# Optimization experiments

Measured on AMD Instinct MI355X. Metric: run time of the kernel, lower is better.

Reference implementation:

```python
import jax, jax.numpy as jnp
import numpy as np

N_EMBD = 768
N_HEAD = 12
HEAD_DIM = N_EMBD // N_HEAD


def setup_inputs() -> dict:
    key = jax.random.key(0)
    k1, k2, k3 = jax.random.split(key, 3)
    B, T, C = 4, 2048, N_EMBD
    x = jax.random.normal(k1, (B, T, C), dtype=jnp.float32)
    # c_attn: torch Linear(C, 3C) -> store as (C, 3C) for x @ W
    w_attn = jax.random.normal(k2, (C, 3 * C), dtype=jnp.float32) * (1.0 / np.sqrt(C))
    b_attn = jax.random.normal(k3, (3 * C,), dtype=jnp.float32) * 0.02
    return {"x": x, "w_attn": w_attn, "b_attn": b_attn}


def reference(x, w_attn, b_attn):
    B, T, C = x.shape
    H, D = N_HEAD, HEAD_DIM
    scale = 1.0 / np.sqrt(D).astype(np.float32)

    qkv = x @ w_attn + b_attn                      # (B, T, 3C)
    q, k, v = jnp.split(qkv, 3, axis=-1)
    q = q.reshape(B, T, H, D).transpose(0, 2, 1, 3)  # (B, H, T, D)
    k = k.reshape(B, T, H, D).transpose(0, 2, 1, 3)
    v = v.reshape(B, T, H, D).transpose(0, 2, 1, 3)

    att = jnp.einsum('bhid,bhjd->bhij', q, k) * scale  # (B, H, T, T)
    causal = jnp.tril(jnp.ones((T, T), dtype=bool))
    # masked positions -> -inf -> relu -> 0; kept positions -> relu(scaled score)
    att = jnp.where(causal, jnp.maximum(att, 0.0), 0.0)

    y = jnp.einsum('bhij,bhjd->bhid', att, v)      # (B, H, T, D)
    y = y.transpose(0, 2, 1, 3).reshape(B, T, C)
    return y
```

## Files before the change

### kernel.cpp

```cpp
#include <hip/hip_runtime.h>
#include <hip/hip_bf16.h>

typedef short bf16x8 __attribute__((ext_vector_type(8)));
typedef float f32x4  __attribute__((ext_vector_type(4)));
typedef unsigned short u16x4 __attribute__((ext_vector_type(4)));

#define CDIM   768
#define NQKV   2304
#define MROWS  8192
#define TSEQ   2048
#define HD     64
#define NHEAD  12
#define BHTOT  48

__device__ __forceinline__ unsigned short f2bf(float f) {
    unsigned int x;
    __builtin_memcpy(&x, &f, 4);
    unsigned int r = (x + 0x7fffu + ((x >> 16) & 1u)) >> 16;
    return (unsigned short)r;
}

__device__ __forceinline__ unsigned int pkbf(float a, float b) {
    unsigned int ua, ub;
    __builtin_memcpy(&ua, &a, 4);
    __builtin_memcpy(&ub, &b, 4);
    return __builtin_amdgcn_perm(ua + 0x8000u, ub + 0x8000u, 0x03020706u);
}

__device__ __forceinline__ f32x4 mfma16(bf16x8 a, bf16x8 b, f32x4 c) {
    return __builtin_amdgcn_mfma_f32_16x16x32_bf16(a, b, c, 0, 0, 0);
}

__device__ __forceinline__ void gl_lds16(const unsigned short* g, unsigned short* l) {
    __builtin_amdgcn_global_load_lds(
        (__attribute__((address_space(1))) void*)(g),
        (__attribute__((address_space(3))) void*)(l),
        16, 0, 0);
}

__global__ __launch_bounds__(256) void convert_x(
    const float* __restrict__ X, unsigned short* __restrict__ Xb)
{
    size_t i = ((size_t)blockIdx.x * 256 + threadIdx.x) * 4;
    f32x4 v = *(const f32x4*)(X + i);
    u16x4 o;
#pragma unroll
    for (int j = 0; j < 4; j++) o[j] = f2bf(v[j]);
    *(u16x4*)(Xb + i) = o;
}

__global__ __launch_bounds__(256) void transpose_w(
    const float* __restrict__ W, unsigned short* __restrict__ Wt)
{
    __shared__ __align__(16) unsigned short tile[64][72];
    const int bx = blockIdx.x;
    const int by = blockIdx.y;
    const int tid = threadIdx.x;
#pragma unroll
    for (int c = 0; c < 4; c++) {
        int chunk = tid + 256 * c;
        int r = chunk >> 4, cc = chunk & 15;
        f32x4 v = *(const f32x4*)(W + (size_t)(by * 64 + r) * NQKV + bx * 64 + cc * 4);
#pragma unroll
        for (int j = 0; j < 4; j++) tile[cc * 4 + j][r] = f2bf(v[j]);
    }
    __syncthreads();
#pragma unroll
    for (int c = 0; c < 2; c++) {
        int chunk = tid + 256 * c;
        int r = chunk >> 3, cc = chunk & 7;
        bf16x8 v;
#pragma unroll
        for (int j = 0; j < 8; j++) v[j] = (short)tile[r][cc * 8 + j];
        *(bf16x8*)(Wt + (size_t)(bx * 64 + r) * CDIM + by * 64 + cc * 8) = v;
    }
}

#define BM 128
#define BN 128
#define BK 64

__global__ __launch_bounds__(256, 4) void qkv_gemm(
    const unsigned short* __restrict__ X,
    const unsigned short* __restrict__ Wt,
    const float* __restrict__ Bias,
    unsigned short* __restrict__ Q,
    unsigned short* __restrict__ Km,
    unsigned short* __restrict__ Vt)
{
    __shared__ __align__(16) unsigned short As[BM * BK];
    __shared__ __align__(16) unsigned short Bs[BN * BK];
    const int tid  = threadIdx.x;
    const int wave = tid >> 6, lane = tid & 63;
    const int quad = lane >> 4, m16 = lane & 15;
    const int wr = wave >> 1, wc = wave & 1;
    const int m0 = blockIdx.y * BM, n0 = blockIdx.x * BN;

    f32x4 acc[4][4];
#pragma unroll
    for (int i = 0; i < 4; i++)
#pragma unroll
        for (int j = 0; j < 4; j++) acc[i][j] = f32x4{0.f, 0.f, 0.f, 0.f};

    const unsigned short* xb = X + (size_t)m0 * CDIM;
    const unsigned short* wb = Wt + (size_t)n0 * CDIM;

    const int srow[4] = {
        (wave * 256 + 0 * 64 + lane) >> 3, (wave * 256 + 1 * 64 + lane) >> 3,
        (wave * 256 + 2 * 64 + lane) >> 3, (wave * 256 + 3 * 64 + lane) >> 3 };
    const int spos = lane & 7;
    const int rb = m16 & 7;

    for (int k0 = 0; k0 < CDIM; k0 += BK) {
#pragma unroll
        for (int c = 0; c < 4; c++) {
            int row = srow[c];
            int ch = spos ^ (row & 7);
            gl_lds16(xb + (size_t)row * CDIM + k0 + ch * 8, As + wave * 2048 + c * 512);
            gl_lds16(wb + (size_t)row * CDIM + k0 + ch * 8, Bs + wave * 2048 + c * 512);
        }
        __syncthreads();
#pragma unroll
        for (int ks = 0; ks < 2; ks++) {
            bf16x8 af[4], bfg[4];
#pragma unroll
            for (int t = 0; t < 4; t++) {
                int rowa = wr * 64 + t * 16 + m16;
                int rowb = wc * 64 + t * 16 + m16;
                int pos = (ks * 4 + quad) ^ rb;
                af[t]  = *(const bf16x8*)(As + rowa * 64 + pos * 8);
                bfg[t] = *(const bf16x8*)(Bs + rowb * 64 + pos * 8);
            }
#pragma unroll
            for (int i = 0; i < 4; i++)
#pragma unroll
                for (int j = 0; j < 4; j++)
                    acc[i][j] = mfma16(af[i], bfg[j], acc[i][j]);
        }
        __syncthreads();
    }

    const int region = n0 / CDIM;
    const float qscale = (region == 0) ? 0.125f : 1.0f;
#pragma unroll
    for (int i = 0; i < 4; i++) {
        int row = m0 + wr * 64 + i * 16 + quad * 4;
#pragma unroll
        for (int j = 0; j < 4; j++) {
            int gcol = n0 + wc * 64 + j * 16 + m16;
            int cc = gcol - region * CDIM;
            int h = cc >> 6, d = cc & 63;
            float bv = Bias[gcol];
#pragma unroll
            for (int r = 0; r < 4; r++) {
                int gm = row + r;
                int b = gm >> 11, t = gm & 2047;
                int bh = b * NHEAD + h;
                unsigned short o = f2bf((acc[i][j][r] + bv) * qscale);
                if (region == 0)      Q[((size_t)bh * TSEQ + t) * HD + d] = o;
                else if (region == 1) Km[((size_t)bh * TSEQ + t) * HD + d] = o;
                else                  Vt[((size_t)bh * HD + d) * TSEQ + t] = o;
            }
        }
    }
}

#define LDSK 0
#define LDSV 8192

__global__ __launch_bounds__(256, 4) void attn(
    const unsigned short* __restrict__ Q,
    const unsigned short* __restrict__ Kmat,
    const unsigned short* __restrict__ Vt,
    float* __restrict__ Out)
{
    __shared__ __align__(16) unsigned short S[16384];

    const int tid  = threadIdx.x;
    const int wave = tid >> 6, lane = tid & 63;
    const int q4 = lane >> 4, m16 = lane & 15;
    const int q8 = m16 >> 2, m3 = m16 & 3;

    const int xcd = blockIdx.x & 7;
    const int idx = blockIdx.x >> 3;
    const int bh  = xcd * 6 + (idx % 6);
    const int it  = 15 - (idx / 6);
    const int i0  = it * 128;

    const unsigned short* qb = Q    + (size_t)bh * TSEQ * HD;
    const unsigned short* kb = Kmat + (size_t)bh * TSEQ * HD;
    const unsigned short* vb = Vt   + (size_t)bh * HD * TSEQ;

    bf16x8 qf[2][2];
#pragma unroll
    for (int si = 0; si < 2; si++)
#pragma unroll
        for (int ks = 0; ks < 2; ks++)
            qf[si][ks] = *(const bf16x8*)(qb +
                (size_t)(i0 + wave * 32 + si * 16 + m16) * HD + ks * 32 + q4 * 8);

    f32x4 oacc[2][4];
#pragma unroll
    for (int si = 0; si < 2; si++)
#pragma unroll
        for (int dn = 0; dn < 4; dn++) oacc[si][dn] = f32x4{0.f, 0.f, 0.f, 0.f};

    const int fr  = ((q8 & 1) << 2) | m3;
    const int kx0 = (q4 ^ fr) * 8;
    const int kx1 = kx0 ^ 32;
    const int krb = (q8 * 8 + m3) * 64;

    for (int jt = 0; jt <= it; jt++) {
        const int j0 = jt * 128;
#pragma unroll
        for (int cc = 0; cc < 4; cc++) {
            int cs = wave * 4 + cc;
            {
                int rowK = cs * 8 + (lane >> 3);
                int chK  = (lane & 7) ^ ((((rowK >> 3) & 1) << 2) | (rowK & 3));
                gl_lds16(kb + (size_t)(j0 + rowK) * HD + chK * 8, &S[LDSK] + cs * 512);
            }
            {
                int dV  = cs * 4 + (lane >> 4);
                int chV = (m16 & 8) | ((m16 ^ dV) & 7);
                gl_lds16(vb + (size_t)dV * TSEQ + j0 + chV * 8, &S[LDSV] + cs * 512);
            }
        }
        __syncthreads();

        const bool diag = (jt == it);
#pragma unroll
        for (int kk = 0; kk < 4; kk++) {
            const int kb0 = kk * 2048 + krb;
            bf16x8 kf_e0 = *(const bf16x8*)(&S[LDSK] + kb0 + kx0);
            bf16x8 kf_e1 = *(const bf16x8*)(&S[LDSK] + kb0 + kx1);
            bf16x8 kf_o0 = *(const bf16x8*)(&S[LDSK] + kb0 + 256 + kx0);
            bf16x8 kf_o1 = *(const bf16x8*)(&S[LDSK] + kb0 + 256 + kx1);

            f32x4 sacc[2][2];
#pragma unroll
            for (int o = 0; o < 2; o++)
#pragma unroll
                for (int si = 0; si < 2; si++) sacc[o][si] = f32x4{0.f, 0.f, 0.f, 0.f};
#pragma unroll
            for (int si = 0; si < 2; si++) {
                sacc[0][si] = mfma16(kf_e0, qf[si][0], sacc[0][si]);
                sacc[0][si] = mfma16(kf_e1, qf[si][1], sacc[0][si]);
                sacc[1][si] = mfma16(kf_o0, qf[si][0], sacc[1][si]);
                sacc[1][si] = mfma16(kf_o1, qf[si][1], sacc[1][si]);
            }

            unsigned int pk[2][2][2];
#pragma unroll
            for (int o = 0; o < 2; o++)
#pragma unroll
                for (int si = 0; si < 2; si++) {
                    f32x4 v = sacc[o][si];
                    if (diag) {
#pragma unroll
                        for (int r = 0; r < 4; r++) {
                            int gj = kk * 32 + q4 * 8 + o * 4 + r;
                            int gi = wave * 32 + si * 16 + m16;
                            if (gj > gi) v[r] = 0.f;
                        }
                    }
#pragma unroll
                    for (int r = 0; r < 4; r++) v[r] = fmaxf(v[r], 0.f);
                    pk[o][si][0] = pkbf(v[0], v[1]);
                    pk[o][si][1] = pkbf(v[2], v[3]);
                }

#pragma unroll
            for (int dn = 0; dn < 4; dn++) {
                int vsw = ((kk * 4 + q4) ^ (m16 & 7)) * 8;
                bf16x8 vf = *(const bf16x8*)(&S[LDSV] + (dn * 16 + m16) * 128 + vsw);
#pragma unroll
                for (int si = 0; si < 2; si++) {
                    union { bf16x8 v; unsigned int u[4]; } af;
                    af.u[0] = pk[0][si][0];
                    af.u[1] = pk[0][si][1];
                    af.u[2] = pk[1][si][0];
                    af.u[3] = pk[1][si][1];
                    oacc[si][dn] = mfma16(af.v, vf, oacc[si][dn]);
                }
            }
        }
        __syncthreads();
    }

    const int b = bh / NHEAD, h = bh % NHEAD;
#pragma unroll
    for (int si = 0; si < 2; si++) {
        int ri = i0 + wave * 32 + si * 16 + q4 * 4;
#pragma unroll
        for (int dn = 0; dn < 4; dn++) {
            int d = dn * 16 + m16;
#pragma unroll
            for (int r = 0; r < 4; r++) {
                Out[((size_t)b * TSEQ + ri + r) * CDIM + h * HD + d] = oacc[si][dn][r];
            }
        }
    }
}

extern "C" void kernel_launch(void* const* d_in, const int* in_sizes, int n_in,
                              void* d_out, int out_size, void* d_ws, size_t ws_size,
                              hipStream_t stream) {
    const float* X    = (const float*)d_in[0];
    const float* W    = (const float*)d_in[1];
    const float* Bias = (const float*)d_in[2];
    float* out = (float*)d_out;

    unsigned short* Xb = (unsigned short*)d_ws;
    unsigned short* Wt = Xb + (size_t)MROWS * CDIM;
    unsigned short* Q  = Wt + (size_t)NQKV * CDIM;
    unsigned short* Km = Q  + (size_t)BHTOT * TSEQ * HD;
    unsigned short* Vt = Km + (size_t)BHTOT * TSEQ * HD;

    hipLaunchKernelGGL(convert_x, dim3((MROWS * CDIM) / 1024), dim3(256), 0, stream, X, Xb);
    hipLaunchKernelGGL(transpose_w, dim3(NQKV / 64, CDIM / 64), dim3(256), 0, stream, W, Wt);
    hipLaunchKernelGGL(qkv_gemm, dim3(NQKV / BN, MROWS / BM), dim3(256), 0, stream,
                       Xb, Wt, Bias, Q, Km, Vt);
    hipLaunchKernelGGL(attn, dim3(BHTOT * 16), dim3(256), 0, stream, Q, Km, Vt, out);
}
```

Baseline: 182.1 us.

## Fuse all stages into one persistent kernel with grid-wide atomic barriers

Merges the input conversion, weight transpose, QKV GEMM and causal attention into a single persistent kernel of 512 blocks, separated by atomic-counter grid barriers instead of separate launches. The attention stage pairs a long and a short query tile in each block so the triangular work is spread more evenly across the fixed grid. This is meant to remove launch gaps and tail imbalance. In exchange it lowers occupancy with launch_bounds(256,2), adds spin-barrier cost, and depends on all 512 blocks being resident at once or the barrier deadlocks.

```diff
diff --git a/kernel.cpp b/kernel.cpp
--- a/kernel.cpp
+++ b/kernel.cpp
@@ -12,6 +12,7 @@
 #define HD     64
 #define NHEAD  12
 #define BHTOT  48
+#define NBLK   512
 
 __device__ __forceinline__ unsigned short f2bf(float f) {
     unsigned int x;
@@ -38,266 +39,281 @@
         16, 0, 0);
 }
 
-__global__ __launch_bounds__(256) void convert_x(
-    const float* __restrict__ X, unsigned short* __restrict__ Xb)
+__device__ __forceinline__ void gbar(unsigned int* ctr) {
+    __syncthreads();
+    if (threadIdx.x == 0) {
+        __threadfence();
+        __hip_atomic_fetch_add(ctr, 1u, __ATOMIC_RELEASE, __HIP_MEMORY_SCOPE_AGENT);
+        while (__hip_atomic_load(ctr, __ATOMIC_ACQUIRE, __HIP_MEMORY_SCOPE_AGENT) <
+               (unsigned)NBLK)
+            __builtin_amdgcn_s_sleep(1);
+        __threadfence();
+    }
+    __syncthreads();
+}
+
+__global__ __launch_bounds__(256, 2) void mega(
+    const float* __restrict__ X, const float* __restrict__ W,
+    const float* __restrict__ Bias, unsigned int* __restrict__ bar,
+    unsigned short* __restrict__ Xb, unsigned short* __restrict__ Wt,
+    unsigned short* __restrict__ Q, unsigned short* __restrict__ Km,
+    unsigned short* __restrict__ Vt, float* __restrict__ Out)
 {
-    size_t i = ((size_t)blockIdx.x * 256 + threadIdx.x) * 4;
-    f32x4 v = *(const f32x4*)(X + i);
-    u16x4 o;
-#pragma unroll
-    for (int j = 0; j < 4; j++) o[j] = f2bf(v[j]);
-    *(u16x4*)(Xb + i) = o;
-}
-
-__global__ __launch_bounds__(256) void transpose_w(
-    const float* __restrict__ W, unsigned short* __restrict__ Wt)
-{
-    __shared__ __align__(16) unsigned short tile[64][72];
-    const int bx = blockIdx.x;
-    const int by = blockIdx.y;
-    const int tid = threadIdx.x;
-#pragma unroll
-    for (int c = 0; c < 4; c++) {
-        int chunk = tid + 256 * c;
-        int r = chunk >> 4, cc = chunk & 15;
-        f32x4 v = *(const f32x4*)(W + (size_t)(by * 64 + r) * NQKV + bx * 64 + cc * 4);
-#pragma unroll
-        for (int j = 0; j < 4; j++) tile[cc * 4 + j][r] = f2bf(v[j]);
-    }
-    __syncthreads();
-#pragma unroll
-    for (int c = 0; c < 2; c++) {
-        int chunk = tid + 256 * c;
-        int r = chunk >> 3, cc = chunk & 7;
-        bf16x8 v;
-#pragma unroll
-        for (int j = 0; j < 8; j++) v[j] = (short)tile[r][cc * 8 + j];
-        *(bf16x8*)(Wt + (size_t)(bx * 64 + r) * CDIM + by * 64 + cc * 8) = v;
-    }
-}
-
-#define BM 128
-#define BN 128
-#define BK 64
-
-__global__ __launch_bounds__(256, 4) void qkv_gemm(
-    const unsigned short* __restrict__ X,
-    const unsigned short* __restrict__ Wt,
-    const float* __restrict__ Bias,
-    unsigned short* __restrict__ Q,
-    unsigned short* __restrict__ Km,
-    unsigned short* __restrict__ Vt)
-{
-    __shared__ __align__(16) unsigned short As[BM * BK];
-    __shared__ __align__(16) unsigned short Bs[BN * BK];
+    __shared__ __align__(16) unsigned short SH[16384];
+
     const int tid  = threadIdx.x;
+    const int blk  = blockIdx.x;
     const int wave = tid >> 6, lane = tid & 63;
     const int quad = lane >> 4, m16 = lane & 15;
-    const int wr = wave >> 1, wc = wave & 1;
-    const int m0 = blockIdx.y * BM, n0 = blockIdx.x * BN;
-
-    f32x4 acc[4][4];
-#pragma unroll
-    for (int i = 0; i < 4; i++)
-#pragma unroll
-        for (int j = 0; j < 4; j++) acc[i][j] = f32x4{0.f, 0.f, 0.f, 0.f};
-
-    const unsigned short* xb = X + (size_t)m0 * CDIM;
-    const unsigned short* wb = Wt + (size_t)n0 * CDIM;
-
-    const int srow[4] = {
-        (wave * 256 + 0 * 64 + lane) >> 3, (wave * 256 + 1 * 64 + lane) >> 3,
-        (wave * 256 + 2 * 64 + lane) >> 3, (wave * 256 + 3 * 64 + lane) >> 3 };
-    const int spos = lane & 7;
-    const int rb = m16 & 7;
-
-    for (int k0 = 0; k0 < CDIM; k0 += BK) {
+
+    if (blk < 432) {
+        unsigned short (*tile)[72] = (unsigned short (*)[72])SH;
+        const int bx = blk % 36, by = blk / 36;
 #pragma unroll
         for (int c = 0; c < 4; c++) {
-            int row = srow[c];
-            int ch = spos ^ (row & 7);
-            gl_lds16(xb + (size_t)row * CDIM + k0 + ch * 8, As + wave * 2048 + c * 512);
-            gl_lds16(wb + (size_t)row * CDIM + k0 + ch * 8, Bs + wave * 2048 + c * 512);
+            int chunk = tid + 256 * c;
+            int r = chunk >> 4, cc = chunk & 15;
+            f32x4 v = *(const f32x4*)(W + (size_t)(by * 64 + r) * NQKV + bx * 64 + cc * 4);
+#pragma unroll
+            for (int j = 0; j < 4; j++) tile[cc * 4 + j][r] = f2bf(v[j]);
         }
         __syncthreads();
 #pragma unroll
-        for (int ks = 0; ks < 2; ks++) {
-            bf16x8 af[4], bfg[4];
-#pragma unroll
-            for (int t = 0; t < 4; t++) {
-                int rowa = wr * 64 + t * 16 + m16;
-                int rowb = wc * 64 + t * 16 + m16;
-                int pos = (ks * 4 + quad) ^ rb;
-                af[t]  = *(const bf16x8*)(As + rowa * 64 + pos * 8);
-                bfg[t] = *(const bf16x8*)(Bs + rowb * 64 + pos * 8);
+        for (int c = 0; c < 2; c++) {
+            int chunk = tid + 256 * c;
+            int r = chunk >> 3, cc = chunk & 7;
+            bf16x8 v;
+#pragma unroll
+            for (int j = 0; j < 8; j++) v[j] = (short)tile[r][cc * 8 + j];
+            *(bf16x8*)(Wt + (size_t)(bx * 64 + r) * CDIM + by * 64 + cc * 8) = v;
+        }
+    }
+#pragma unroll 1
+    for (int c = 0; c < 12; c++) {
+        size_t i4 = (size_t)c * NBLK * 256 + (size_t)blk * 256 + tid;
+        f32x4 v = *(const f32x4*)(X + i4 * 4);
+        u16x4 o;
+#pragma unroll
+        for (int j = 0; j < 4; j++) o[j] = f2bf(v[j]);
+        *(u16x4*)(Xb + i4 * 4) = o;
+    }
+    gbar(&bar[0]);
+
+    {
+        unsigned short* As = SH;
+        unsigned short* Bs = SH + 8192;
+        const int wr = wave >> 1, wc = wave & 1;
+        const int srow[4] = {
+            (wave * 256 + 0 * 64 + lane) >> 3, (wave * 256 + 1 * 64 + lane) >> 3,
+            (wave * 256 + 2 * 64 + lane) >> 3, (wave * 256 + 3 * 64 + lane) >> 3 };
+        const int spos = lane & 7;
+        const int rb = m16 & 7;
+        const int ntile = (blk < 128) ? 3 : 2;
+
+#pragma unroll 1
+        for (int tt = 0; tt < ntile; tt++) {
+            const int t = blk + tt * NBLK;
+            const int xcd = t & 7, s = t >> 3;
+            const int m0 = (xcd * 8 + (s & 7)) * 128;
+            const int n0 = (s >> 3) * 128;
+
+            f32x4 acc[4][4];
+#pragma unroll
+            for (int i = 0; i < 4; i++)
+#pragma unroll
+                for (int j = 0; j < 4; j++) acc[i][j] = f32x4{0.f, 0.f, 0.f, 0.f};
+
+            const unsigned short* xb = Xb + (size_t)m0 * CDIM;
+            const unsigned short* wb = Wt + (size_t)n0 * CDIM;
+
+            for (int k0 = 0; k0 < CDIM; k0 += 64) {
+#pragma unroll
+                for (int c = 0; c < 4; c++) {
+                    int row = srow[c];
+                    int ch = spos ^ (row & 7);
+                    gl_lds16(xb + (size_t)row * CDIM + k0 + ch * 8, As + wave * 2048 + c * 512);
+                    gl_lds16(wb + (size_t)row * CDIM + k0 + ch * 8, Bs + wave * 2048 + c * 512);
+                }
+                __syncthreads();
+#pragma unroll
+                for (int ks = 0; ks < 2; ks++) {
+                    bf16x8 af[4], bfg[4];
+#pragma unroll
+                    for (int u = 0; u < 4; u++) {
+                        int rowa = wr * 64 + u * 16 + m16;
+                        int rowb = wc * 64 + u * 16 + m16;
+                        int pos = (ks * 4 + quad) ^ rb;
+                        af[u]  = *(const bf16x8*)(As + rowa * 64 + pos * 8);
+                        bfg[u] = *(const bf16x8*)(Bs + rowb * 64 + pos * 8);
+                    }
+#pragma unroll
+                    for (int i = 0; i < 4; i++)
+#pragma unroll
+                        for (int j = 0; j < 4; j++)
+                            acc[i][j] = mfma16(af[i], bfg[j], acc[i][j]);
+                }
+                __syncthreads();
             }
-#pragma unroll
-            for (int i = 0; i < 4; i++)
-#pragma unroll
-                for (int j = 0; j < 4; j++)
-                    acc[i][j] = mfma16(af[i], bfg[j], acc[i][j]);
-        }
-        __syncthreads();
-    }
-
-    const int region = n0 / CDIM;
-    const float qscale = (region == 0) ? 0.125f : 1.0f;
-#pragma unroll
-    for (int i = 0; i < 4; i++) {
-        int row = m0 + wr * 64 + i * 16 + quad * 4;
-#pragma unroll
-        for (int j = 0; j < 4; j++) {
-            int gcol = n0 + wc * 64 + j * 16 + m16;
-            int cc = gcol - region * CDIM;
-            int h = cc >> 6, d = cc & 63;
-            float bv = Bias[gcol];
-#pragma unroll
-            for (int r = 0; r < 4; r++) {
-                int gm = row + r;
-                int b = gm >> 11, t = gm & 2047;
-                int bh = b * NHEAD + h;
-                unsigned short o = f2bf((acc[i][j][r] + bv) * qscale);
-                if (region == 0)      Q[((size_t)bh * TSEQ + t) * HD + d] = o;
-                else if (region == 1) Km[((size_t)bh * TSEQ + t) * HD + d] = o;
-                else                  Vt[((size_t)bh * HD + d) * TSEQ + t] = o;
+
+            const int region = n0 / CDIM;
+            const float qscale = (region == 0) ? 0.125f : 1.0f;
+#pragma unroll
+            for (int i = 0; i < 4; i++) {
+                int row = m0 + wr * 64 + i * 16 + quad * 4;
+#pragma unroll
+                for (int j = 0; j < 4; j++) {
+                    int gcol = n0 + wc * 64 + j * 16 + m16;
+                    int cc = gcol - region * CDIM;
+                    int h = cc >> 6, d = cc & 63;
+                    float bv = Bias[gcol];
+#pragma unroll
+                    for (int r = 0; r < 4; r++) {
+                        int gm = row + r;
+                        int b = gm >> 11, tq = gm & 2047;
+                        int bh = b * NHEAD + h;
+                        unsigned short o = f2bf((acc[i][j][r] + bv) * qscale);
+                        if (region == 0)      Q[((size_t)bh * TSEQ + tq) * HD + d] = o;
+                        else if (region == 1) Km[((size_t)bh * TSEQ + tq) * HD + d] = o;
+                        else                  Vt[((size_t)bh * HD + d) * TSEQ + tq] = o;
+                    }
+                }
             }
         }
     }
-}
-
-#define LDSK 0
-#define LDSV 8192
-
-__global__ __launch_bounds__(256, 4) void attn(
-    const unsigned short* __restrict__ Q,
-    const unsigned short* __restrict__ Kmat,
-    const unsigned short* __restrict__ Vt,
-    float* __restrict__ Out)
-{
-    __shared__ __align__(16) unsigned short S[16384];
-
-    const int tid  = threadIdx.x;
-    const int wave = tid >> 6, lane = tid & 63;
-    const int q4 = lane >> 4, m16 = lane & 15;
-    const int q8 = m16 >> 2, m3 = m16 & 3;
-
-    const int xcd = blockIdx.x & 7;
-    const int idx = blockIdx.x >> 3;
-    const int bh  = xcd * 6 + (idx % 6);
-    const int it  = 15 - (idx / 6);
-    const int i0  = it * 128;
-
-    const unsigned short* qb = Q    + (size_t)bh * TSEQ * HD;
-    const unsigned short* kb = Kmat + (size_t)bh * TSEQ * HD;
-    const unsigned short* vb = Vt   + (size_t)bh * HD * TSEQ;
-
-    bf16x8 qf[2][2];
-#pragma unroll
-    for (int si = 0; si < 2; si++)
-#pragma unroll
-        for (int ks = 0; ks < 2; ks++)
-            qf[si][ks] = *(const bf16x8*)(qb +
-                (size_t)(i0 + wave * 32 + si * 16 + m16) * HD + ks * 32 + q4 * 8);
-
-    f32x4 oacc[2][4];
-#pragma unroll
-    for (int si = 0; si < 2; si++)
-#pragma unroll
-        for (int dn = 0; dn < 4; dn++) oacc[si][dn] = f32x4{0.f, 0.f, 0.f, 0.f};
-
-    const int fr  = ((q8 & 1) << 2) | m3;
-    const int kx0 = (q4 ^ fr) * 8;
-    const int kx1 = kx0 ^ 32;
-    const int krb = (q8 * 8 + m3) * 64;
-
-    for (int jt = 0; jt <= it; jt++) {
-        const int j0 = jt * 128;
-#pragma unroll
-        for (int cc = 0; cc < 4; cc++) {
-            int cs = wave * 4 + cc;
-            {
-                int rowK = cs * 8 + (lane >> 3);
-                int chK  = (lane & 7) ^ ((((rowK >> 3) & 1) << 2) | (rowK & 3));
-                gl_lds16(kb + (size_t)(j0 + rowK) * HD + chK * 8, &S[LDSK] + cs * 512);
+    gbar(&bar[1]);
+
+    {
+        unsigned short* SK = SH;
+        unsigned short* SV = SH + 8192;
+        const int q4 = quad, q8 = m16 >> 2, m3 = m16 & 3;
+
+        const int xcd = blk & 7, u = blk >> 3;
+        int jb_it[2], nj = 0, bh = 0;
+        if (u < 60) {
+            bh = xcd * 6 + u / 10;
+            int r = u % 10;
+            if (r < 4) { jb_it[0] = 15 - r; jb_it[1] = 0; nj = 1; }
+            else       { int p = r - 4; jb_it[0] = 11 - p; jb_it[1] = p; nj = 2; }
+        }
+
+        const int fr  = ((q8 & 1) << 2) | m3;
+        const int kx0 = (q4 ^ fr) * 8;
+        const int kx1 = kx0 ^ 32;
+        const int krb = (q8 * 8 + m3) * 64;
+
+        const unsigned short* qb = Q  + (size_t)bh * TSEQ * HD;
+        const unsigned short* kb = Km + (size_t)bh * TSEQ * HD;
+        const unsigned short* vb = Vt + (size_t)bh * HD * TSEQ;
+
+#pragma unroll 1
+        for (int jj = 0; jj < nj; jj++) {
+            const int it = jb_it[jj];
+            const int i0 = it * 128;
+
+            bf16x8 qf[2][2];
+#pragma unroll
+            for (int si = 0; si < 2; si++)
+#pragma unroll
+                for (int ks = 0; ks < 2; ks++)
+                    qf[si][ks] = *(const bf16x8*)(qb +
+                        (size_t)(i0 + wave * 32 + si * 16 + m16) * HD + ks * 32 + q4 * 8);
+
+            f32x4 oacc[2][4];
+#pragma unroll
+            for (int si = 0; si < 2; si++)
+#pragma unroll
+                for (int dn = 0; dn < 4; dn++) oacc[si][dn] = f32x4{0.f, 0.f, 0.f, 0.f};
+
+            for (int jt = 0; jt <= it; jt++) {
+                const int j0 = jt * 128;
+#pragma unroll
+                for (int cc = 0; cc < 4; cc++) {
+                    int cs = wave * 4 + cc;
+                    {
+                        int rowK = cs * 8 + (lane >> 3);
+                        int chK  = (lane & 7) ^ ((((rowK >> 3) & 1) << 2) | (rowK & 3));
+                        gl_lds16(kb + (size_t)(j0 + rowK) * HD + chK * 8, SK + cs * 512);
+                    }
+                    {
+                        int dV  = cs * 4 + (lane >> 4);
+                        int chV = (m16 & 8) | ((m16 ^ dV) & 7);
+                        gl_lds16(vb + (size_t)dV * TSEQ + j0 + chV * 8, SV + cs * 512);
+                    }
+                }
+                __syncthreads();
+
+                const bool diag = (jt == it);
+#pragma unroll
+                for (int kk = 0; kk < 4; kk++) {
+                    const int kb0 = kk * 2048 + krb;
+                    bf16x8 kf_e0 = *(const bf16x8*)(SK + kb0 + kx0);
+                    bf16x8 kf_e1 = *(const bf16x8*)(SK + kb0 + kx1);
+                    bf16x8 kf_o0 = *(const bf16x8*)(SK + kb0 + 256 + kx0);
+                    bf16x8 kf_o1 = *(const bf16x8*)(SK + kb0 + 256 + kx1);
+
+                    f32x4 sacc[2][2];
+#pragma unroll
+                    for (int o = 0; o < 2; o++)
+#pragma unroll
+                        for (int si = 0; si < 2; si++) sacc[o][si] = f32x4{0.f, 0.f, 0.f, 0.f};
+#pragma unroll
+                    for (int si = 0; si < 2; si++) {
+                        sacc[0][si] = mfma16(kf_e0, qf[si][0], sacc[0][si]);
+                        sacc[0][si] = mfma16(kf_e1, qf[si][1], sacc[0][si]);
+                        sacc[1][si] = mfma16(kf_o0, qf[si][0], sacc[1][si]);
+                        sacc[1][si] = mfma16(kf_o1, qf[si][1], sacc[1][si]);
+                    }
+
+                    unsigned int pk[2][2][2];
+#pragma unroll
+                    for (int o = 0; o < 2; o++)
+#pragma unroll
+                        for (int si = 0; si < 2; si++) {
+                            f32x4 v = sacc[o][si];
+                            if (diag) {
+#pragma unroll
+                                for (int r = 0; r < 4; r++) {
+                                    int gj = kk * 32 + q4 * 8 + o * 4 + r;
+                                    int gi = wave * 32 + si * 16 + m16;
+                                    if (gj > gi) v[r] = 0.f;
+                                }
+                            }
+#pragma unroll
+                            for (int r = 0; r < 4; r++) v[r] = fmaxf(v[r], 0.f);
+                            pk[o][si][0] = pkbf(v[0], v[1]);
+                            pk[o][si][1] = pkbf(v[2], v[3]);
+                        }
+
+#pragma unroll
+                    for (int dn = 0; dn < 4; dn++) {
+                        int vsw = ((kk * 4 + q4) ^ (m16 & 7)) * 8;
+                        bf16x8 vf = *(const bf16x8*)(SV + (dn * 16 + m16) * 128 + vsw);
+#pragma unroll
+                        for (int si = 0; si < 2; si++) {
+                            union { bf16x8 v; unsigned int uu[4]; } af;
+                            af.uu[0] = pk[0][si][0];
+                            af.uu[1] = pk[0][si][1];
+                            af.uu[2] = pk[1][si][0];
+                            af.uu[3] = pk[1][si][1];
+                            oacc[si][dn] = mfma16(af.v, vf, oacc[si][dn]);
+                        }
+                    }
+                }
+                __syncthreads();
             }
-            {
-                int dV  = cs * 4 + (lane >> 4);
-                int chV = (m16 & 8) | ((m16 ^ dV) & 7);
-                gl_lds16(vb + (size_t)dV * TSEQ + j0 + chV * 8, &S[LDSV] + cs * 512);
-            }
-        }
-        __syncthreads();
-
-        const bool diag = (jt == it);
-#pragma unroll
-        for (int kk = 0; kk < 4; kk++) {
-            const int kb0 = kk * 2048 + krb;
-            bf16x8 kf_e0 = *(const bf16x8*)(&S[LDSK] + kb0 + kx0);
-            bf16x8 kf_e1 = *(const bf16x8*)(&S[LDSK] + kb0 + kx1);
-            bf16x8 kf_o0 = *(const bf16x8*)(&S[LDSK] + kb0 + 256 + kx0);
-            bf16x8 kf_o1 = *(const bf16x8*)(&S[LDSK] + kb0 + 256 + kx1);
-
-            f32x4 sacc[2][2];
-#pragma unroll
-            for (int o = 0; o < 2; o++)
-#pragma unroll
-                for (int si = 0; si < 2; si++) sacc[o][si] = f32x4{0.f, 0.f, 0.f, 0.f};
+
+            const int b = bh / NHEAD, h = bh % NHEAD;
 #pragma unroll
             for (int si = 0; si < 2; si++) {
-                sacc[0][si] = mfma16(kf_e0, qf[si][0], sacc[0][si]);
-                sacc[0][si] = mfma16(kf_e1, qf[si][1], sacc[0][si]);
-                sacc[1][si] = mfma16(kf_o0, qf[si][0], sacc[1][si]);
-                sacc[1][si] = mfma16(kf_o1, qf[si][1], sacc[1][si]);
-            }
-
-            unsigned int pk[2][2][2];
-#pragma unroll
-            for (int o = 0; o < 2; o++)
-#pragma unroll
-                for (int si = 0; si < 2; si++) {
-                    f32x4 v = sacc[o][si];
-                    if (diag) {
-#pragma unroll
-                        for (int r = 0; r < 4; r++) {
-                            int gj = kk * 32 + q4 * 8 + o * 4 + r;
-                            int gi = wave * 32 + si * 16 + m16;
-                            if (gj > gi) v[r] = 0.f;
-                        }
-                    }
-#pragma unroll
-                    for (int r = 0; r < 4; r++) v[r] = fmaxf(v[r], 0.f);
-                    pk[o][si][0] = pkbf(v[0], v[1]);
-                    pk[o][si][1] = pkbf(v[2], v[3]);
-                }
-
-#pragma unroll
-            for (int dn = 0; dn < 4; dn++) {
-                int vsw = ((kk * 4 + q4) ^ (m16 & 7)) * 8;
-                bf16x8 vf = *(const bf16x8*)(&S[LDSV] + (dn * 16 + m16) * 128 + vsw);
-#pragma unroll
-                for (int si = 0; si < 2; si++) {
-                    union { bf16x8 v; unsigned int u[4]; } af;
-                    af.u[0] = pk[0][si][0];
-                    af.u[1] = pk[0][si][1];
-                    af.u[2] = pk[1][si][0];
-                    af.u[3] = pk[1][si][1];
-                    oacc[si][dn] = mfma16(af.v, vf, oacc[si][dn]);
-                }
-            }
-        }
-        __syncthreads();
-    }
-
-    const int b = bh / NHEAD, h = bh % NHEAD;
-#pragma unroll
-    for (int si = 0; si < 2; si++) {
-        int ri = i0 + wave * 32 + si * 16 + q4 * 4;
-#pragma unroll
-        for (int dn = 0; dn < 4; dn++) {
-            int d = dn * 16 + m16;
-#pragma unroll
-            for (int r = 0; r < 4; r++) {
-                Out[((size_t)b * TSEQ + ri + r) * CDIM + h * HD + d] = oacc[si][dn][r];
+                int ri = i0 + wave * 32 + si * 16 + q4 * 4;
+#pragma unroll
+                for (int dn = 0; dn < 4; dn++) {
+                    int d = dn * 16 + m16;
+#pragma unroll
+                    for (int r = 0; r < 4; r++) {
+                        Out[((size_t)b * TSEQ + ri + r) * CDIM + h * HD + d] = oacc[si][dn][r];
+                    }
+                }
             }
         }
     }
@@ -311,15 +327,14 @@
     const float* Bias = (const float*)d_in[2];
     float* out = (float*)d_out;
 
-    unsigned short* Xb = (unsigned short*)d_ws;
-    unsigned short* Wt = Xb + (size_t)MROWS * CDIM;
-    unsigned short* Q  = Wt + (size_t)NQKV * CDIM;
-    unsigned short* Km = Q  + (size_t)BHTOT * TSEQ * HD;
-    unsigned short* Vt = Km + (size_t)BHTOT * TSEQ * HD;
-
-    hipLaunchKernelGGL(convert_x, dim3((MROWS * CDIM) / 1024), dim3(256), 0, stream, X, Xb);
-    hipLaunchKernelGGL(transpose_w, dim3(NQKV / 64, CDIM / 64), dim3(256), 0, stream, W, Wt);
-    hipLaunchKernelGGL(qkv_gemm, dim3(NQKV / BN, MROWS / BM), dim3(256), 0, stream,
-                       Xb, Wt, Bias, Q, Km, Vt);
-    hipLaunchKernelGGL(attn, dim3(BHTOT * 16), dim3(256), 0, stream, Q, Km, Vt, out);
-}
+    unsigned int*   bar = (unsigned int*)d_ws;
+    unsigned short* Xb  = (unsigned short*)d_ws + 32;
+    unsigned short* Wt  = Xb + (size_t)MROWS * CDIM;
+    unsigned short* Q   = Wt + (size_t)NQKV * CDIM;
+    unsigned short* Km  = Q  + (size_t)BHTOT * TSEQ * HD;
+    unsigned short* Vt  = Km + (size_t)BHTOT * TSEQ * HD;
+
+    hipMemsetAsync(bar, 0, 64, stream);
+    hipLaunchKernelGGL(mega, dim3(NBLK), dim3(256), 0, stream,
+                       X, W, Bias, bar, Xb, Wt, Q, Km, Vt, out);
+}
```

Result: slower. 490.5 us (+169.4%).

## Merge prep kernels and enlarge QKV GEMM tile with XCD-aware block mapping

Applied to the files above, without the earlier changes.

Folds the fp32-to-bf16 conversion of X and the transpose of W into one persistent prep kernel, which removes a launch. The QKV GEMM moves to 512-thread blocks with a 256x128 tile, so each W tile is reused across more rows. Blocks are remapped so each XCD gets a contiguous set of M rows, which should improve L2 locality. The cost is a larger LDS footprint per block and a launch_bounds of 512 threads with 4 blocks, which may limit occupancy or register allocation.

```diff
diff --git a/kernel.cpp b/kernel.cpp
--- a/kernel.cpp
+++ b/kernel.cpp
@@ -38,49 +38,46 @@
         16, 0, 0);
 }
 
-__global__ __launch_bounds__(256) void convert_x(
-    const float* __restrict__ X, unsigned short* __restrict__ Xb)
+__global__ __launch_bounds__(256) void prep(
+    const float* __restrict__ X, const float* __restrict__ W,
+    unsigned short* __restrict__ Xb, unsigned short* __restrict__ Wt)
 {
-    size_t i = ((size_t)blockIdx.x * 256 + threadIdx.x) * 4;
-    f32x4 v = *(const f32x4*)(X + i);
-    u16x4 o;
-#pragma unroll
-    for (int j = 0; j < 4; j++) o[j] = f2bf(v[j]);
-    *(u16x4*)(Xb + i) = o;
-}
-
-__global__ __launch_bounds__(256) void transpose_w(
-    const float* __restrict__ W, unsigned short* __restrict__ Wt)
-{
-    __shared__ __align__(16) unsigned short tile[64][72];
-    const int bx = blockIdx.x;
-    const int by = blockIdx.y;
-    const int tid = threadIdx.x;
-#pragma unroll
-    for (int c = 0; c < 4; c++) {
-        int chunk = tid + 256 * c;
-        int r = chunk >> 4, cc = chunk & 15;
-        f32x4 v = *(const f32x4*)(W + (size_t)(by * 64 + r) * NQKV + bx * 64 + cc * 4);
-#pragma unroll
-        for (int j = 0; j < 4; j++) tile[cc * 4 + j][r] = f2bf(v[j]);
-    }
-    __syncthreads();
-#pragma unroll
-    for (int c = 0; c < 2; c++) {
-        int chunk = tid + 256 * c;
-        int r = chunk >> 3, cc = chunk & 7;
-        bf16x8 v;
-#pragma unroll
-        for (int j = 0; j < 8; j++) v[j] = (short)tile[r][cc * 8 + j];
-        *(bf16x8*)(Wt + (size_t)(bx * 64 + r) * CDIM + by * 64 + cc * 8) = v;
-    }
-}
-
-#define BM 128
-#define BN 128
+    const int tid = threadIdx.x, blk = blockIdx.x;
+    if (blk < 432) {
+        __shared__ __align__(16) unsigned short tile[64][72];
+        const int bx = blk % 36, by = blk / 36;
+#pragma unroll
+        for (int c = 0; c < 4; c++) {
+            int chunk = tid + 256 * c;
+            int r = chunk >> 4, cc = chunk & 15;
+            f32x4 v = *(const f32x4*)(W + (size_t)(by * 64 + r) * NQKV + bx * 64 + cc * 4);
+#pragma unroll
+            for (int j = 0; j < 4; j++) tile[cc * 4 + j][r] = f2bf(v[j]);
+        }
+        __syncthreads();
+#pragma unroll
+        for (int c = 0; c < 2; c++) {
+            int chunk = tid + 256 * c;
+            int r = chunk >> 3, cc = chunk & 7;
+            bf16x8 v;
+#pragma unroll
+            for (int j = 0; j < 8; j++) v[j] = (short)tile[r][cc * 8 + j];
+            *(bf16x8*)(Wt + (size_t)(bx * 64 + r) * CDIM + by * 64 + cc * 8) = v;
+        }
+    }
+    for (size_t i4 = (size_t)blk * 256 + tid; i4 < (size_t)(MROWS * CDIM / 4);
+         i4 += (size_t)448 * 256) {
+        f32x4 v = *(const f32x4*)(X + i4 * 4);
+        u16x4 o;
+#pragma unroll
+        for (int j = 0; j < 4; j++) o[j] = f2bf(v[j]);
+        *(u16x4*)(Xb + i4 * 4) = o;
+    }
+}
+
 #define BK 64
 
-__global__ __launch_bounds__(256, 4) void qkv_gemm(
+__global__ __launch_bounds__(512, 4) void qkv_gemm(
     const unsigned short* __restrict__ X,
     const unsigned short* __restrict__ Wt,
     const float* __restrict__ Bias,
@@ -88,13 +85,17 @@
     unsigned short* __restrict__ Km,
     unsigned short* __restrict__ Vt)
 {
-    __shared__ __align__(16) unsigned short As[BM * BK];
-    __shared__ __align__(16) unsigned short Bs[BN * BK];
+    __shared__ __align__(16) unsigned short As[256 * BK];
+    __shared__ __align__(16) unsigned short Bs[128 * BK];
     const int tid  = threadIdx.x;
     const int wave = tid >> 6, lane = tid & 63;
     const int quad = lane >> 4, m16 = lane & 15;
     const int wr = wave >> 1, wc = wave & 1;
-    const int m0 = blockIdx.y * BM, n0 = blockIdx.x * BN;
+
+    const int t   = blockIdx.x;
+    const int xcd = t & 7, s = t >> 3;
+    const int m0  = (xcd * 4 + (s & 3)) * 256;
+    const int n0  = (s >> 2) * 128;
 
     f32x4 acc[4][4];
 #pragma unroll
@@ -105,31 +106,36 @@
     const unsigned short* xb = X + (size_t)m0 * CDIM;
     const unsigned short* wb = Wt + (size_t)n0 * CDIM;
 
-    const int srow[4] = {
-        (wave * 256 + 0 * 64 + lane) >> 3, (wave * 256 + 1 * 64 + lane) >> 3,
-        (wave * 256 + 2 * 64 + lane) >> 3, (wave * 256 + 3 * 64 + lane) >> 3 };
     const int spos = lane & 7;
     const int rb = m16 & 7;
+    int arow[4], brow[2];
+#pragma unroll
+    for (int c = 0; c < 4; c++) arow[c] = (wave * 256 + c * 64 + lane) >> 3;
+#pragma unroll
+    for (int c = 0; c < 2; c++) brow[c] = (wave * 128 + c * 64 + lane) >> 3;
 
     for (int k0 = 0; k0 < CDIM; k0 += BK) {
 #pragma unroll
         for (int c = 0; c < 4; c++) {
-            int row = srow[c];
-            int ch = spos ^ (row & 7);
+            int row = arow[c], ch = spos ^ (row & 7);
             gl_lds16(xb + (size_t)row * CDIM + k0 + ch * 8, As + wave * 2048 + c * 512);
-            gl_lds16(wb + (size_t)row * CDIM + k0 + ch * 8, Bs + wave * 2048 + c * 512);
+        }
+#pragma unroll
+        for (int c = 0; c < 2; c++) {
+            int row = brow[c], ch = spos ^ (row & 7);
+            gl_lds16(wb + (size_t)row * CDIM + k0 + ch * 8, Bs + wave * 1024 + c * 512);
         }
         __syncthreads();
 #pragma unroll
         for (int ks = 0; ks < 2; ks++) {
             bf16x8 af[4], bfg[4];
 #pragma unroll
-            for (int t = 0; t < 4; t++) {
-                int rowa = wr * 64 + t * 16 + m16;
-                int rowb = wc * 64 + t * 16 + m16;
+            for (int u = 0; u < 4; u++) {
+                int rowa = wr * 64 + u * 16 + m16;
+                int rowb = wc * 64 + u * 16 + m16;
                 int pos = (ks * 4 + quad) ^ rb;
-                af[t]  = *(const bf16x8*)(As + rowa * 64 + pos * 8);
-                bfg[t] = *(const bf16x8*)(Bs + rowb * 64 + pos * 8);
+                af[u]  = *(const bf16x8*)(As + rowa * 64 + pos * 8);
+                bfg[u] = *(const bf16x8*)(Bs + rowb * 64 + pos * 8);
             }
 #pragma unroll
             for (int i = 0; i < 4; i++)
@@ -154,12 +160,12 @@
 #pragma unroll
             for (int r = 0; r < 4; r++) {
                 int gm = row + r;
-                int b = gm >> 11, t = gm & 2047;
+                int b = gm >> 11, tq = gm & 2047;
                 int bh = b * NHEAD + h;
                 unsigned short o = f2bf((acc[i][j][r] + bv) * qscale);
-                if (region == 0)      Q[((size_t)bh * TSEQ + t) * HD + d] = o;
-                else if (region == 1) Km[((size_t)bh * TSEQ + t) * HD + d] = o;
-                else                  Vt[((size_t)bh * HD + d) * TSEQ + t] = o;
+                if (region == 0)      Q[((size_t)bh * TSEQ + tq) * HD + d] = o;
+                else if (region == 1) Km[((size_t)bh * TSEQ + tq) * HD + d] = o;
+                else                  Vt[((size_t)bh * HD + d) * TSEQ + tq] = o;
             }
         }
     }
@@ -317,9 +323,8 @@
     unsigned short* Km = Q  + (size_t)BHTOT * TSEQ * HD;
     unsigned short* Vt = Km + (size_t)BHTOT * TSEQ * HD;
 
-    hipLaunchKernelGGL(convert_x, dim3((MROWS * CDIM) / 1024), dim3(256), 0, stream, X, Xb);
-    hipLaunchKernelGGL(transpose_w, dim3(NQKV / 64, CDIM / 64), dim3(256), 0, stream, W, Wt);
-    hipLaunchKernelGGL(qkv_gemm, dim3(NQKV / BN, MROWS / BM), dim3(256), 0, stream,
+    hipLaunchKernelGGL(prep, dim3(448), dim3(256), 0, stream, X, W, Xb, Wt);
+    hipLaunchKernelGGL(qkv_gemm, dim3(576), dim3(512), 0, stream,
                        Xb, Wt, Bias, Q, Km, Vt);
     hipLaunchKernelGGL(attn, dim3(BHTOT * 16), dim3(256), 0, stream, Q, Km, Vt, out);
 }
```

Result: faster. 178.0 us (-2.3%).
